# Performance work log

Measured on AMD Instinct MI355X. Metric: run time of the kernel, lower is better.

## Reference

```python
import jax, jax.numpy as jnp
import numpy as np

H = 16
D_MODEL = 1024
D_K = D_MODEL // H


def setup_inputs() -> dict:
    key = jax.random.key(0)
    ks = jax.random.split(key, 12)
    B, S = 2, 2048
    scale = 1.0 / np.sqrt(D_MODEL)
    inp = {
        "query": jax.random.normal(ks[0], (B, S, D_MODEL), jnp.float32),
        "key": jax.random.normal(ks[1], (B, S, D_MODEL), jnp.float32),
        "value": jax.random.normal(ks[2], (B, S, D_MODEL), jnp.float32),
        "mask": jnp.ones((B, 1, S), jnp.int32),
        "Wq": jax.random.normal(ks[3], (D_MODEL, D_MODEL), jnp.float32) * scale,
        "bq": jnp.zeros((D_MODEL,), jnp.float32),
        "Wk": jax.random.normal(ks[4], (D_MODEL, D_MODEL), jnp.float32) * scale,
        "bk": jnp.zeros((D_MODEL,), jnp.float32),
        "Wv": jax.random.normal(ks[5], (D_MODEL, D_MODEL), jnp.float32) * scale,
        "bv": jnp.zeros((D_MODEL,), jnp.float32),
        "Wo": jax.random.normal(ks[6], (D_MODEL, D_MODEL), jnp.float32) * scale,
        "bo": jnp.zeros((D_MODEL,), jnp.float32),
    }
    return inp


def reference(query, key, value, mask, Wq, bq, Wk, bk, Wv, bv, Wo, bo):
    B, S, _ = query.shape
    # QKV projections, split heads: [B, S, D] -> [B, H, S, d_k]
    def proj(x, W, b):
        y = x @ W.T + b
        return y.reshape(B, -1, H, D_K).transpose(0, 2, 1, 3)

    q = proj(query, Wq, bq)
    k = proj(key, Wk, bk)
    v = proj(value, Wv, bv)

    # scaled dot-product attention with full score matrix [B, H, Sq, Sk]
    scores = jnp.einsum("bhqd,bhkd->bhqk", q, k) / np.sqrt(D_K)
    m = mask[:, None, :, :]  # unsqueeze head dim: [B, 1, 1_or_S, S]
    scores = jnp.where(m == 0, jnp.float32(-1e9), scores)
    p_attn = jax.nn.softmax(scores, axis=-1)  # dropout p=0.0 (eval)
    x = jnp.einsum("bhqk,bhkd->bhqd", p_attn, v)

    # merge heads and output projection
    x = x.transpose(0, 2, 1, 3).reshape(B, -1, H * D_K)
    return x @ Wo.T + bo
```

## Files before the change

### kernel.cpp

```cpp
#include <hip/hip_runtime.h>
#include <hip/hip_bf16.h>
#include <stdint.h>

typedef unsigned short us;
typedef __bf16 bf8 __attribute__((ext_vector_type(8)));
typedef float  f4  __attribute__((ext_vector_type(4)));

typedef unsigned int __attribute__((address_space(1))) as1_uint;
typedef unsigned int __attribute__((address_space(3))) as3_uint;

__device__ __forceinline__ void async_ld16(const void* g, void* l) {
    __builtin_amdgcn_global_load_lds((as1_uint*)g, (as3_uint*)l, 16, 0, 0);
}

__device__ __forceinline__ us f2bf(float f) {
    __hip_bfloat16 h = __float2bfloat16(f);
    us u;
    __builtin_memcpy(&u, &h, 2);
    return u;
}

__device__ __forceinline__ unsigned pack2bf(float a, float b) {
    __hip_bfloat162 h2 = __float22bfloat162_rn(make_float2(a, b));
    unsigned u;
    __builtin_memcpy(&u, &h2, 4);
    return u;
}

__device__ __forceinline__ float fexp2(float x) {
#if __has_builtin(__builtin_amdgcn_exp2f)
    return __builtin_amdgcn_exp2f(x);
#else
    return exp2f(x);
#endif
}

#define SCALE_Q 0.18033688011112042f

__global__ __launch_bounds__(256)
void convert_all(const float* __restrict__ s0, const float* __restrict__ s1,
                 const float* __restrict__ s2, const float* __restrict__ s3,
                 const float* __restrict__ s4, const float* __restrict__ s5,
                 const float* __restrict__ s6,
                 us* __restrict__ d0, us* __restrict__ d1, us* __restrict__ d2,
                 us* __restrict__ d3, us* __restrict__ d4, us* __restrict__ d5,
                 us* __restrict__ d6)
{
    size_t i4 = (((size_t)blockIdx.x * 256) + threadIdx.x) << 2;
    const float* src; us* dst; size_t off;
    if (i4 < ((size_t)3 << 22)) {
        unsigned seg = (unsigned)(i4 >> 22);
        off = i4 & (((size_t)1 << 22) - 1);
        src = seg == 0 ? s0 : (seg == 1 ? s1 : s2);
        dst = seg == 0 ? d0 : (seg == 1 ? d1 : d2);
    } else {
        size_t j = i4 - ((size_t)3 << 22);
        unsigned seg = (unsigned)(j >> 20);
        off = j & (((size_t)1 << 20) - 1);
        src = seg == 0 ? s3 : (seg == 1 ? s4 : (seg == 2 ? s5 : s6));
        dst = seg == 0 ? d3 : (seg == 1 ? d4 : (seg == 2 ? d5 : d6));
    }
    float4 f = *(const float4*)(src + off);
    ushort4 o;
    o.x = f2bf(f.x); o.y = f2bf(f.y); o.z = f2bf(f.z); o.w = f2bf(f.w);
    *(ushort4*)(dst + off) = o;
}

template<int MODE, int BN>
__device__ __forceinline__
void gemm_body(const us* __restrict__ A, const us* __restrict__ W,
               const float* __restrict__ bias, void* __restrict__ out,
               float scale, int bx, int by)
{
    __shared__ us lA[128 * 32];
    __shared__ us lB[BN * 32];

    const int tid  = threadIdx.x;
    const int wv   = tid >> 6;
    const int lane = tid & 63;
    const int l15  = lane & 15;
    const int quad = lane >> 4;
    const int kq   = quad << 3;
    const int cr   = quad << 2;
    const int srow = lane >> 2;
    const int scol = (lane & 3) << 3;
    const int m0   = by << 7;
    const int n0   = bx * BN;
    constexpr int MJ = (BN == 128) ? 4 : 2;
    const int wm = (BN == 128) ? ((wv >> 1) << 6) : (wv << 5);
    const int wn = (BN == 128) ? ((wv & 1) << 6) : 0;

    f4 acc[4][MJ];
    const f4 zero = {0.f, 0.f, 0.f, 0.f};
#pragma unroll
    for (int i = 0; i < 4; ++i)
#pragma unroll
        for (int j = 0; j < MJ; ++j) acc[i][j] = zero;

    for (int kt = 0; kt < 1024; kt += 32) {
#pragma unroll
        for (int s = 0; s < 2; ++s) {
            const int chunk = wv * 2 + s;
            const int row   = chunk * 16 + srow;
            async_ld16(A + (size_t)(m0 + row) * 1024 + kt + scol, &lA[chunk * 512]);
        }
        if (BN == 128) {
#pragma unroll
            for (int s = 0; s < 2; ++s) {
                const int chunk = wv * 2 + s;
                const int row   = chunk * 16 + srow;
                async_ld16(W + (size_t)(n0 + row) * 1024 + kt + scol, &lB[chunk * 512]);
            }
        } else {
            const int row = wv * 16 + srow;
            async_ld16(W + (size_t)(n0 + row) * 1024 + kt + scol, &lB[wv * 512]);
        }
        __syncthreads();

        bf8 wf[4], xf[MJ];
#pragma unroll
        for (int i = 0; i < 4; ++i)
            wf[i] = *(const bf8*)&lB[(wn + i * 16 + l15) * 32 + kq];
#pragma unroll
        for (int j = 0; j < MJ; ++j)
            xf[j] = *(const bf8*)&lA[(wm + j * 16 + l15) * 32 + kq];
#pragma unroll
        for (int i = 0; i < 4; ++i)
#pragma unroll
            for (int j = 0; j < MJ; ++j)
                acc[i][j] = __builtin_amdgcn_mfma_f32_16x16x32_bf16(wf[i], xf[j], acc[i][j], 0, 0, 0);
        __syncthreads();
    }

    if (MODE == 2) {
        us* o = (us*)out;
#pragma unroll
        for (int j = 0; j < MJ; ++j) {
            const int f = m0 + wm + j * 16 + l15;
            const float bf_ = bias[f];
            const int hh = f >> 6, dd = f & 63;
#pragma unroll
            for (int i = 0; i < 4; ++i) {
                const int tokb = n0 + wn + i * 16 + cr;
                const int bb2 = tokb >> 11, ss = tokb & 2047;
                uint2 w;
                w.x = pack2bf(acc[i][j][0] + bf_, acc[i][j][1] + bf_);
                w.y = pack2bf(acc[i][j][2] + bf_, acc[i][j][3] + bf_);
                *(uint2*)&o[((size_t)((bb2 * 16 + hh) * 64 + dd) << 11) + ss] = w;
            }
        }
        return;
    }

#pragma unroll
    for (int i = 0; i < 4; ++i) {
        const int gnb = n0 + wn + i * 16 + cr;
        const f4 bj = *(const f4*)&bias[gnb];
        if (MODE == 0) {
            us* o = (us*)out;
            const int hh = gnb >> 6, dd = gnb & 63;
#pragma unroll
            for (int j = 0; j < MJ; ++j) {
                const int gm = m0 + wm + j * 16 + l15;
                const int bb2 = gm >> 11, ss = gm & 2047;
                uint2 w;
                w.x = pack2bf((acc[i][j][0] + bj[0]) * scale, (acc[i][j][1] + bj[1]) * scale);
                w.y = pack2bf((acc[i][j][2] + bj[2]) * scale, (acc[i][j][3] + bj[3]) * scale);
                *(uint2*)&o[(((size_t)(bb2 * 16 + hh) * 2048 + ss) << 6) + dd] = w;
            }
        } else {
            float* o = (float*)out;
#pragma unroll
            for (int j = 0; j < MJ; ++j) {
                const int gm = m0 + wm + j * 16 + l15;
                f4 v;
#pragma unroll
                for (int r = 0; r < 4; ++r) v[r] = acc[i][j][r] + bj[r];
                *(f4*)&o[((size_t)gm << 10) + gnb] = v;
            }
        }
    }
}

__global__ __launch_bounds__(256)
void gemm_qkv(const us* __restrict__ XQ, const us* __restrict__ XK,
              const us* __restrict__ XV,
              const us* __restrict__ WQ, const us* __restrict__ WK,
              const us* __restrict__ WV,
              const float* __restrict__ bq, const float* __restrict__ bk,
              const float* __restrict__ bv,
              us* __restrict__ QP, us* __restrict__ KP, us* __restrict__ VT)
{
    const int z = blockIdx.z;
    if (z == 2) {
        gemm_body<2, 128>(WV, XV, bv, VT, 1.0f, blockIdx.y, blockIdx.x);
        return;
    }
    const us* A = z == 0 ? XQ : XK;
    const us* W = z == 0 ? WQ : WK;
    const float* b = z == 0 ? bq : bk;
    us* o = z == 0 ? QP : KP;
    const float scale = z == 0 ? SCALE_Q : 1.0f;
    gemm_body<0, 128>(A, W, b, o, scale, blockIdx.x, blockIdx.y);
}

__global__ __launch_bounds__(256)
void gemm_o(const us* __restrict__ A, const us* __restrict__ W,
            const float* __restrict__ bias, float* __restrict__ out)
{
    gemm_body<1, 64>(A, W, bias, out, 1.0f, blockIdx.x, blockIdx.y);
}

__global__ __launch_bounds__(256)
void flash_attn(const us* __restrict__ Qp, const us* __restrict__ Kp,
                const us* __restrict__ Vtp, const int* __restrict__ maskp,
                us* __restrict__ ctx)
{
    __shared__ us lK[64 * 64];
    __shared__ us lVt[64 * 64];
    __shared__ us lP[4 * 32 * 72];

    const int tid  = threadIdx.x;
    const int wv   = tid >> 6;
    const int lane = tid & 63;
    const int l15  = lane & 15;
    const int quad = lane >> 4;
    const int cr   = quad << 2;
    const int l7   = l15 & 7;

    const int q0 = blockIdx.x << 7;
    const int h  = blockIdx.y;
    const int b  = blockIdx.z;

    const size_t headoff = ((size_t)(b * 16 + h)) << 17;
    const us* Qh  = Qp  + headoff;
    const us* Kh  = Kp  + headoff;
    const us* Vth = Vtp + headoff;
    const int* mrow = maskp + ((size_t)b << 11);

    bf8 qf[2][2];
#pragma unroll
    for (int nt = 0; nt < 2; ++nt)
#pragma unroll
        for (int kb = 0; kb < 2; ++kb)
            qf[nt][kb] = *(const bf8*)(Qh + ((size_t)(q0 + wv * 32 + nt * 16 + l15) << 6)
                                          + kb * 32 + (quad << 3));

    const f4 zero = {0.f, 0.f, 0.f, 0.f};
    f4 of[4][2];
#pragma unroll
    for (int dt = 0; dt < 4; ++dt)
#pragma unroll
        for (int nt = 0; nt < 2; ++nt) of[dt][nt] = zero;
    float li[2] = {0.f, 0.f};

    us* lPw = lP + wv * (32 * 72);

    const int sr = lane >> 3;
    const int sc = lane & 7;

    for (int kt0 = 0; kt0 < 2048; kt0 += 64) {
        __syncthreads();

#pragma unroll
        for (int it = 0; it < 2; ++it) {
            const int r = wv * 16 + it * 8 + sr;
            const int sw = (sc ^ (r & 7)) << 3;
            uint4 kv = *(const uint4*)(Kh + ((size_t)(kt0 + r) << 6) + sc * 8);
            *(uint4*)&lK[(r << 6) + sw] = kv;
            uint4 vv = *(const uint4*)(Vth + ((size_t)r << 11) + kt0 + sc * 8);
            *(uint4*)&lVt[(r << 6) + sw] = vv;
        }
        __syncthreads();

        float rs[2] = {0.f, 0.f};
#pragma unroll
        for (int kt = 0; kt < 4; ++kt) {
            const int krow = (kt * 16 + l15) << 6;
            bf8 kf0 = *(const bf8*)&lK[krow + ((quad ^ l7) << 3)];
            bf8 kf1 = *(const bf8*)&lK[krow + (((4 + quad) ^ l7) << 3)];
            f4 st[2];
#pragma unroll
            for (int nt = 0; nt < 2; ++nt) {
                st[nt] = __builtin_amdgcn_mfma_f32_16x16x32_bf16(kf0, qf[nt][0], zero, 0, 0, 0);
                st[nt] = __builtin_amdgcn_mfma_f32_16x16x32_bf16(kf1, qf[nt][1], st[nt], 0, 0, 0);
            }
            const int4 m4 = *(const int4*)(mrow + kt0 + kt * 16 + cr);
            f4 mr;
            mr[0] = m4.x ? 1.0f : 0.0f;
            mr[1] = m4.y ? 1.0f : 0.0f;
            mr[2] = m4.z ? 1.0f : 0.0f;
            mr[3] = m4.w ? 1.0f : 0.0f;
#pragma unroll
            for (int nt = 0; nt < 2; ++nt) {
                float p0 = fexp2(st[nt][0]) * mr[0];
                float p1 = fexp2(st[nt][1]) * mr[1];
                float p2 = fexp2(st[nt][2]) * mr[2];
                float p3 = fexp2(st[nt][3]) * mr[3];
                rs[nt] += (p0 + p1) + (p2 + p3);
                uint2 w;
                w.x = pack2bf(p0, p1);
                w.y = pack2bf(p2, p3);
                *(uint2*)&lPw[(nt * 16 + l15) * 72 + kt * 16 + cr] = w;
            }
        }
#pragma unroll
        for (int nt = 0; nt < 2; ++nt) {
            float r2 = rs[nt];
            r2 += __shfl_xor(r2, 16, 64);
            r2 += __shfl_xor(r2, 32, 64);
            li[nt] += r2;
        }

#pragma unroll
        for (int kb = 0; kb < 2; ++kb) {
            bf8 pfr[2];
#pragma unroll
            for (int nt = 0; nt < 2; ++nt)
                pfr[nt] = *(const bf8*)&lPw[(nt * 16 + l15) * 72 + kb * 32 + (quad << 3)];
#pragma unroll
            for (int dt = 0; dt < 4; ++dt) {
                bf8 vf = *(const bf8*)&lVt[((dt * 16 + l15) << 6) + (((kb * 4 + quad) ^ l7) << 3)];
#pragma unroll
                for (int nt = 0; nt < 2; ++nt)
                    of[dt][nt] = __builtin_amdgcn_mfma_f32_16x16x32_bf16(vf, pfr[nt], of[dt][nt], 0, 0, 0);
            }
        }
    }

#pragma unroll
    for (int nt = 0; nt < 2; ++nt) {
        const float linv = 1.0f / li[nt];
        const int tok = q0 + wv * 32 + nt * 16 + l15;
        const size_t rowb = (((size_t)(b * 2048 + tok)) << 10) + (h << 6);
#pragma unroll
        for (int dt = 0; dt < 4; ++dt) {
            uint2 w;
            w.x = pack2bf(of[dt][nt][0] * linv, of[dt][nt][1] * linv);
            w.y = pack2bf(of[dt][nt][2] * linv, of[dt][nt][3] * linv);
            *(uint2*)&ctx[rowb + dt * 16 + cr] = w;
        }
    }
}

extern "C" void kernel_launch(void* const* d_in, const int* in_sizes, int n_in,
                              void* d_out, int out_size, void* d_ws, size_t ws_size,
                              hipStream_t stream)
{
    const float* q    = (const float*)d_in[0];
    const float* k    = (const float*)d_in[1];
    const float* v    = (const float*)d_in[2];
    const int*   mask = (const int*)d_in[3];
    const float* Wq   = (const float*)d_in[4];
    const float* bq   = (const float*)d_in[5];
    const float* Wk   = (const float*)d_in[6];
    const float* bk   = (const float*)d_in[7];
    const float* Wv   = (const float*)d_in[8];
    const float* bv   = (const float*)d_in[9];
    const float* Wo   = (const float*)d_in[10];
    const float* bo   = (const float*)d_in[11];
    float* out = (float*)d_out;

    us* ws  = (us*)d_ws;
    us* XQ  = ws;
    us* XK  = ws + 4194304;
    us* XV  = ws + 8388608;
    us* WQb = ws + 12582912;
    us* WKb = ws + 13631488;
    us* WVb = ws + 14680064;
    us* WOb = ws + 15728640;
    us* QP  = ws + 16777216;
    us* KP  = ws + 20971520;
    us* VT  = ws + 25165824;
    us* CTX = XQ;

    convert_all<<<16384, 256, 0, stream>>>(q, k, v, Wq, Wk, Wv, Wo,
                                           XQ, XK, XV, WQb, WKb, WVb, WOb);
    gemm_qkv<<<dim3(8, 32, 3), 256, 0, stream>>>(XQ, XK, XV, WQb, WKb, WVb,
                                                 bq, bk, bv, QP, KP, VT);
    flash_attn<<<dim3(16, 16, 2), 256, 0, stream>>>(QP, KP, VT, mask, CTX);
    gemm_o<<<dim3(16, 32), 256, 0, stream>>>(CTX, WOb, bo, out);
}
```

Before: 283.7 us.

## Split attention key range across wave pairs with LDS reduction of partial outputs

The flash attention kernel now assigns each wave 64 query rows and half of the key sequence, where it previously handled 32 query rows over the full key sequence. Each K tile is loaded for both key halves at once, and the partial outputs and row sums are combined through shared memory at the end. The intent is to halve the number of serial key-loop iterations and reuse each K/V fragment across more query rows per MFMA. In exchange, register use (accumulators and Q fragments double) and shared memory (about 68 KB) go up, which may lower occupancy.

```diff
diff --git a/kernel.cpp b/kernel.cpp
--- a/kernel.cpp
+++ b/kernel.cpp
@@ -216,9 +216,12 @@
                 const us* __restrict__ Vtp, const int* __restrict__ maskp,
                 us* __restrict__ ctx)
 {
-    __shared__ us lK[64 * 64];
-    __shared__ us lVt[64 * 64];
-    __shared__ us lP[4 * 32 * 72];
+    __shared__ char smem[69632];
+    us* lK  = (us*)smem;
+    us* lVt = (us*)(smem + 16384);
+    us* lP  = (us*)(smem + 32768);
+    float* red = (float*)smem;
+    float* liR = (float*)(smem + 34816);
 
     const int tid  = threadIdx.x;
     const int wv   = tid >> 6;
@@ -227,6 +230,8 @@
     const int quad = lane >> 4;
     const int cr   = quad << 2;
     const int l7   = l15 & 7;
+    const int qh   = wv & 1;
+    const int kh   = wv >> 1;
 
     const int q0 = blockIdx.x << 7;
     const int h  = blockIdx.y;
@@ -238,61 +243,66 @@
     const us* Vth = Vtp + headoff;
     const int* mrow = maskp + ((size_t)b << 11);
 
-    bf8 qf[2][2];
-#pragma unroll
-    for (int nt = 0; nt < 2; ++nt)
+    us* lKh  = lK  + kh * 4096;
+    us* lVth = lVt + kh * 4096;
+    us* lPw  = lP + wv * (64 * 72);
+
+    bf8 qf[4][2];
+#pragma unroll
+    for (int nt = 0; nt < 4; ++nt)
 #pragma unroll
         for (int kb = 0; kb < 2; ++kb)
-            qf[nt][kb] = *(const bf8*)(Qh + ((size_t)(q0 + wv * 32 + nt * 16 + l15) << 6)
+            qf[nt][kb] = *(const bf8*)(Qh + ((size_t)(q0 + qh * 64 + nt * 16 + l15) << 6)
                                           + kb * 32 + (quad << 3));
 
     const f4 zero = {0.f, 0.f, 0.f, 0.f};
-    f4 of[4][2];
+    f4 of[4][4];
 #pragma unroll
     for (int dt = 0; dt < 4; ++dt)
 #pragma unroll
-        for (int nt = 0; nt < 2; ++nt) of[dt][nt] = zero;
-    float li[2] = {0.f, 0.f};
-
-    us* lPw = lP + wv * (32 * 72);
-
-    const int sr = lane >> 3;
-    const int sc = lane & 7;
-
-    for (int kt0 = 0; kt0 < 2048; kt0 += 64) {
+        for (int nt = 0; nt < 4; ++nt) of[dt][nt] = zero;
+    float li[4] = {0.f, 0.f, 0.f, 0.f};
+
+    const int sr = tid >> 3;
+    const int sc = tid & 7;
+
+    for (int kt0 = 0; kt0 < 1024; kt0 += 64) {
         __syncthreads();
 
 #pragma unroll
-        for (int it = 0; it < 2; ++it) {
-            const int r = wv * 16 + it * 8 + sr;
-            const int sw = (sc ^ (r & 7)) << 3;
-            uint4 kv = *(const uint4*)(Kh + ((size_t)(kt0 + r) << 6) + sc * 8);
-            *(uint4*)&lK[(r << 6) + sw] = kv;
-            uint4 vv = *(const uint4*)(Vth + ((size_t)r << 11) + kt0 + sc * 8);
-            *(uint4*)&lVt[(r << 6) + sw] = vv;
+        for (int hf = 0; hf < 2; ++hf) {
+#pragma unroll
+            for (int it = 0; it < 2; ++it) {
+                const int r = it * 32 + sr;
+                const int sw = (sc ^ (r & 7)) << 3;
+                uint4 kv = *(const uint4*)(Kh + ((size_t)(hf * 1024 + kt0 + r) << 6) + sc * 8);
+                *(uint4*)&lK[hf * 4096 + (r << 6) + sw] = kv;
+                uint4 vv = *(const uint4*)(Vth + ((size_t)r << 11) + hf * 1024 + kt0 + sc * 8);
+                *(uint4*)&lVt[hf * 4096 + (r << 6) + sw] = vv;
+            }
         }
         __syncthreads();
 
-        float rs[2] = {0.f, 0.f};
+        float rs[4] = {0.f, 0.f, 0.f, 0.f};
 #pragma unroll
         for (int kt = 0; kt < 4; ++kt) {
             const int krow = (kt * 16 + l15) << 6;
-            bf8 kf0 = *(const bf8*)&lK[krow + ((quad ^ l7) << 3)];
-            bf8 kf1 = *(const bf8*)&lK[krow + (((4 + quad) ^ l7) << 3)];
-            f4 st[2];
-#pragma unroll
-            for (int nt = 0; nt < 2; ++nt) {
+            bf8 kf0 = *(const bf8*)&lKh[krow + ((quad ^ l7) << 3)];
+            bf8 kf1 = *(const bf8*)&lKh[krow + (((4 + quad) ^ l7) << 3)];
+            f4 st[4];
+#pragma unroll
+            for (int nt = 0; nt < 4; ++nt) {
                 st[nt] = __builtin_amdgcn_mfma_f32_16x16x32_bf16(kf0, qf[nt][0], zero, 0, 0, 0);
                 st[nt] = __builtin_amdgcn_mfma_f32_16x16x32_bf16(kf1, qf[nt][1], st[nt], 0, 0, 0);
             }
-            const int4 m4 = *(const int4*)(mrow + kt0 + kt * 16 + cr);
+            const int4 m4 = *(const int4*)(mrow + kh * 1024 + kt0 + kt * 16 + cr);
             f4 mr;
             mr[0] = m4.x ? 1.0f : 0.0f;
             mr[1] = m4.y ? 1.0f : 0.0f;
             mr[2] = m4.z ? 1.0f : 0.0f;
             mr[3] = m4.w ? 1.0f : 0.0f;
 #pragma unroll
-            for (int nt = 0; nt < 2; ++nt) {
+            for (int nt = 0; nt < 4; ++nt) {
                 float p0 = fexp2(st[nt][0]) * mr[0];
                 float p1 = fexp2(st[nt][1]) * mr[1];
                 float p2 = fexp2(st[nt][2]) * mr[2];
@@ -305,7 +315,7 @@
             }
         }
 #pragma unroll
-        for (int nt = 0; nt < 2; ++nt) {
+        for (int nt = 0; nt < 4; ++nt) {
             float r2 = rs[nt];
             r2 += __shfl_xor(r2, 16, 64);
             r2 += __shfl_xor(r2, 32, 64);
@@ -314,31 +324,49 @@
 
 #pragma unroll
         for (int kb = 0; kb < 2; ++kb) {
-            bf8 pfr[2];
-#pragma unroll
-            for (int nt = 0; nt < 2; ++nt)
+            bf8 pfr[4];
+#pragma unroll
+            for (int nt = 0; nt < 4; ++nt)
                 pfr[nt] = *(const bf8*)&lPw[(nt * 16 + l15) * 72 + kb * 32 + (quad << 3)];
 #pragma unroll
             for (int dt = 0; dt < 4; ++dt) {
-                bf8 vf = *(const bf8*)&lVt[((dt * 16 + l15) << 6) + (((kb * 4 + quad) ^ l7) << 3)];
-#pragma unroll
-                for (int nt = 0; nt < 2; ++nt)
+                bf8 vf = *(const bf8*)&lVth[((dt * 16 + l15) << 6) + (((kb * 4 + quad) ^ l7) << 3)];
+#pragma unroll
+                for (int nt = 0; nt < 4; ++nt)
                     of[dt][nt] = __builtin_amdgcn_mfma_f32_16x16x32_bf16(vf, pfr[nt], of[dt][nt], 0, 0, 0);
             }
         }
     }
 
-#pragma unroll
-    for (int nt = 0; nt < 2; ++nt) {
-        const float linv = 1.0f / li[nt];
-        const int tok = q0 + wv * 32 + nt * 16 + l15;
-        const size_t rowb = (((size_t)(b * 2048 + tok)) << 10) + (h << 6);
-#pragma unroll
-        for (int dt = 0; dt < 4; ++dt) {
-            uint2 w;
-            w.x = pack2bf(of[dt][nt][0] * linv, of[dt][nt][1] * linv);
-            w.y = pack2bf(of[dt][nt][2] * linv, of[dt][nt][3] * linv);
-            *(uint2*)&ctx[rowb + dt * 16 + cr] = w;
+    __syncthreads();
+    if (kh == 1) {
+#pragma unroll
+        for (int nt = 0; nt < 4; ++nt)
+#pragma unroll
+            for (int dt = 0; dt < 4; ++dt)
+                *(f4*)&red[(qh * 64 + nt * 16 + l15) * 68 + dt * 16 + cr] = of[dt][nt];
+        if (quad == 0) {
+#pragma unroll
+            for (int nt = 0; nt < 4; ++nt)
+                liR[qh * 64 + nt * 16 + l15] = li[nt];
+        }
+    }
+    __syncthreads();
+    if (kh == 0) {
+#pragma unroll
+        for (int nt = 0; nt < 4; ++nt) {
+            const float lt = li[nt] + liR[qh * 64 + nt * 16 + l15];
+            const float linv = 1.0f / lt;
+            const int tok = q0 + qh * 64 + nt * 16 + l15;
+            const size_t rowb = (((size_t)(b * 2048 + tok)) << 10) + (h << 6);
+#pragma unroll
+            for (int dt = 0; dt < 4; ++dt) {
+                const f4 o2 = *(const f4*)&red[(qh * 64 + nt * 16 + l15) * 68 + dt * 16 + cr];
+                uint2 w;
+                w.x = pack2bf((of[dt][nt][0] + o2[0]) * linv, (of[dt][nt][1] + o2[1]) * linv);
+                w.y = pack2bf((of[dt][nt][2] + o2[2]) * linv, (of[dt][nt][3] + o2[3]) * linv);
+                *(uint2*)&ctx[rowb + dt * 16 + cr] = w;
+            }
         }
     }
 }
```

After: 270.3 us. 1.05x faster.
